# Kernel optimization log

Measured on AMD Instinct MI355X. Metric: run time of the kernel, lower is better.

The kernel has to match this reference:

```python
import jax, jax.numpy as jnp
import numpy as np

N = 100000      # nodes
E = 1600000     # edges
F_IN = 64       # CFG.feature_dim
H = 128         # CFG.hidden_dim
G = 128         # graphs in batch
LN_EPS = 1e-5


def setup_inputs() -> dict:
    key = jax.random.key(0)
    ks = jax.random.split(key, 12)
    x = jax.random.normal(ks[0], (N, F_IN), dtype=jnp.float32)
    edge_index = jax.random.randint(ks[1], (2, E), 0, N)
    batch = jnp.sort(jax.random.randint(ks[2], (N,), 0, G))
    # GCNConv weights (glorot-ish scale) and biases
    W1 = jax.random.normal(ks[3], (F_IN, H), dtype=jnp.float32) * (1.0 / np.sqrt(F_IN))
    b1 = jnp.zeros((H,), jnp.float32)
    W2 = jax.random.normal(ks[4], (H, H), dtype=jnp.float32) * (1.0 / np.sqrt(H))
    b2 = jnp.zeros((H,), jnp.float32)
    # LayerNorm affine params
    g1 = jnp.ones((H,), jnp.float32)
    beta1 = jnp.zeros((H,), jnp.float32)
    g2 = jnp.ones((H,), jnp.float32)
    beta2 = jnp.zeros((H,), jnp.float32)
    return {"x": x, "edge_index": edge_index, "batch": batch,
            "W1": W1, "b1": b1, "g1": g1, "beta1": beta1,
            "W2": W2, "b2": b2, "g2": g2, "beta2": beta2,
            "num_graphs": G}


def _gcn_conv(h, W, b, src, dst, n):
    """PyG GCNConv: add self-loops, symmetric D^-1/2 (A+I) D^-1/2 (h W) + b."""
    hw = h @ W                                   # [n, out]
    loop = jnp.arange(n, dtype=src.dtype)
    s = jnp.concatenate([src, loop])             # [E+n]
    d = jnp.concatenate([dst, loop])
    deg = jax.ops.segment_sum(jnp.ones_like(s, jnp.float32), d, num_segments=n)
    dinv = jax.lax.rsqrt(jnp.maximum(deg, 1e-12))
    norm = dinv[s] * dinv[d]                     # [E+n]
    msg = hw[s] * norm[:, None]                  # gather + scale
    out = jax.ops.segment_sum(msg, d, num_segments=n)
    return out + b


def _layer_norm(h, gamma, beta):
    mu = jnp.mean(h, axis=-1, keepdims=True)
    var = jnp.mean(jnp.square(h - mu), axis=-1, keepdims=True)
    return (h - mu) * jax.lax.rsqrt(var + LN_EPS) * gamma + beta


def reference(x, edge_index, batch, W1, b1, g1, beta1, W2, b2, g2, beta2, num_graphs):
    src, dst = edge_index[0], edge_index[1]
    n = x.shape[0]
    h = _gcn_conv(x, W1, b1, src, dst, n)
    h = _layer_norm(h, g1, beta1)
    h = jax.nn.relu(h)
    h = _gcn_conv(h, W2, b2, src, dst, n)
    h = _layer_norm(h, g2, beta2)
    # is_inverted defaults to False -> no sign flip
    sums = jax.ops.segment_sum(h, batch, num_segments=num_graphs)      # [G, H]
    counts = jax.ops.segment_sum(jnp.ones((n,), jnp.float32), batch, num_segments=num_graphs)
    return sums / jnp.maximum(counts, 1.0)[:, None]
```

## Files before the change

### kernel.cpp

```cpp
#include <hip/hip_runtime.h>

#define LN_EPS 1e-5f

typedef __attribute__((ext_vector_type(8))) short short8v;
typedef __attribute__((ext_vector_type(4))) float float4v;

__device__ __forceinline__ float bflo(unsigned u) { return __uint_as_float(u << 16); }
__device__ __forceinline__ float bfhi(unsigned u) { return __uint_as_float(u & 0xffff0000u); }
__device__ __forceinline__ unsigned short f2bf(float f) {
    unsigned b = __float_as_uint(f);
    unsigned r = b + 0x7fffu + ((b >> 16) & 1u);
    return (unsigned short)(r >> 16);
}
__device__ __forceinline__ unsigned pack2(float x, float y) {
    return (unsigned)f2bf(x) | ((unsigned)f2bf(y) << 16);
}
__device__ __forceinline__ void add8(float* a, uint4 u) {
    a[0] += bflo(u.x); a[1] += bfhi(u.x);
    a[2] += bflo(u.y); a[3] += bfhi(u.y);
    a[4] += bflo(u.z); a[5] += bfhi(u.z);
    a[6] += bflo(u.w); a[7] += bfhi(u.w);
}

union U4S8 { uint4 u; short8v s; };


#define CHUNK 4096
#define NBMAX 512
#define CSRCAP 8192

__launch_bounds__(256)
__global__ void k_bcnt(const int* __restrict__ dst, int e, int* __restrict__ bcnt) {
    __shared__ int hist[NBMAX];
    int tid = threadIdx.x;
    int c0 = blockIdx.x * CHUNK;
    if (c0 >= e) return;
    int cnt = min(CHUNK, e - c0);
    for (int t = tid; t < NBMAX; t += 256) hist[t] = 0;
    __syncthreads();
    for (int t = tid; t < cnt; t += 256)
        atomicAdd(&hist[((unsigned)dst[c0 + t]) >> 8], 1);
    __syncthreads();
    for (int b = tid; b < NBMAX; b += 256) {
        int h = hist[b];
        if (h > 0) atomicAdd(&bcnt[b], h);
    }
}

__launch_bounds__(512)
__global__ void k_bscan(const int* __restrict__ bcnt, int* __restrict__ bptr) {
    __shared__ int s[NBMAX];
    int tid = threadIdx.x;
    int v = bcnt[tid];
    s[tid] = v; __syncthreads();
    for (int o = 1; o < NBMAX; o <<= 1) {
        int t = (tid >= o) ? s[tid - o] : 0;
        __syncthreads();
        s[tid] += t;
        __syncthreads();
    }
    bptr[tid + 1] = s[tid];
    if (tid == 0) bptr[0] = 0;
}

__launch_bounds__(256)
__global__ void k_bucket(const int* __restrict__ src, const int* __restrict__ dst, int e,
                         const int* __restrict__ bptr, int* __restrict__ gcnt,
                         uint2* __restrict__ stage) {
    __shared__ uint2 ebuf[CHUNK];
    __shared__ int hist[NBMAX];
    __shared__ int base[NBMAX];
    int tid = threadIdx.x;
    int c0 = blockIdx.x * CHUNK;
    if (c0 >= e) return;
    int cnt = min(CHUNK, e - c0);

    for (int t = tid; t < NBMAX; t += 256) hist[t] = 0;
    __syncthreads();
    for (int t = tid; t < cnt; t += 256) {
        uint2 ed = make_uint2((unsigned)src[c0 + t], (unsigned)dst[c0 + t]);
        ebuf[t] = ed;
        atomicAdd(&hist[ed.y >> 8], 1);
    }
    __syncthreads();
    for (int b = tid; b < NBMAX; b += 256) {
        int h = hist[b];
        if (h > 0) base[b] = bptr[b] + atomicAdd(&gcnt[b], h);
    }
    __syncthreads();
    for (int t = tid; t < cnt; t += 256) {
        uint2 ed = ebuf[t];
        int p = atomicAdd(&base[ed.y >> 8], 1);
        stage[p] = ed;
    }
}

__launch_bounds__(256)
__global__ void k_csr(const uint2* __restrict__ stage, const int* __restrict__ bptr,
                      int* __restrict__ csr_src, int* __restrict__ row_ptr,
                      float* __restrict__ dinv, int n, int e) {
    __shared__ int cntl[256];
    __shared__ int sc[256];
    __shared__ int excl[256];
    __shared__ int cbuf[CSRCAP];
    int b = blockIdx.x;
    int lo = b << 8;
    int nn = min(n - lo, 256);
    int tid = threadIdx.x;
    int s0 = bptr[b], s1 = bptr[b + 1];
    int cntB = s1 - s0;

    cntl[tid] = 0;
    __syncthreads();
    for (int t = tid; t < cntB; t += 256) {
        int dl = (int)stage[s0 + t].y - lo;
        atomicAdd(&cntl[dl], 1);
    }
    __syncthreads();
    int deg = (tid < nn) ? cntl[tid] : 0;
    sc[tid] = deg; __syncthreads();
    for (int o = 1; o < 256; o <<= 1) {
        int t = (tid >= o) ? sc[tid - o] : 0;
        __syncthreads();
        sc[tid] += t;
        __syncthreads();
    }
    excl[tid] = sc[tid] - deg;
    if (tid < nn) {
        row_ptr[lo + tid] = s0 + excl[tid];
        dinv[lo + tid] = rsqrtf((float)(deg + 1));
    }
    if (b == 0 && tid == 0) row_ptr[n] = e;
    cntl[tid] = 0;
    __syncthreads();
    for (int t = tid; t < cntB; t += 256) {
        uint2 ed = stage[s0 + t];
        int dl = (int)ed.y - lo;
        int r = atomicAdd(&cntl[dl], 1);
        int p = excl[dl] + r;
        if (p < CSRCAP) cbuf[p] = (int)ed.x;
        else csr_src[s0 + p] = (int)ed.x;
    }
    __syncthreads();
    int lim = min(cntB, CSRCAP);
    for (int t = tid; t < lim; t += 256) csr_src[s0 + t] = cbuf[t];
}


__global__ void k_f2bs(const float* __restrict__ in, const float* __restrict__ dinv,
                       unsigned* __restrict__ out, int nu) {
    int i = blockIdx.x * blockDim.x + threadIdx.x;
    if (i < nu) {
        float2 v = ((const float2*)in)[i];
        float d = dinv[i >> 5];
        out[i] = pack2(v.x * d, v.y * d);
    }
}


__global__ void k_agg64b(const uint4* __restrict__ x4, const float* __restrict__ dinv,
                         const int* __restrict__ row_ptr, const int* __restrict__ csr_src,
                         uint4* __restrict__ out4, int n) {
    int lane = threadIdx.x & 63;
    int g = lane >> 3, c = lane & 7;
    int wid = (blockIdx.x * blockDim.x + threadIdx.x) >> 6;
    int nw = (gridDim.x * blockDim.x) >> 6;
    for (int i = wid; i < n; i += nw) {
        float a[8] = {0.f, 0.f, 0.f, 0.f, 0.f, 0.f, 0.f, 0.f};
        if (g == 0) {
            uint4 su = x4[(size_t)i * 8 + c];
            add8(a, su);
        }
        int j0 = row_ptr[i], j1 = row_ptr[i + 1];
        int j = j0 + g;
        for (; j + 8 < j1; j += 16) {
            int s0 = csr_src[j], s1 = csr_src[j + 8];
            uint4 u0 = x4[(size_t)s0 * 8 + c];
            uint4 u1 = x4[(size_t)s1 * 8 + c];
            add8(a, u0);
            add8(a, u1);
        }
        if (j < j1) {
            int s0 = csr_src[j];
            uint4 u0 = x4[(size_t)s0 * 8 + c];
            add8(a, u0);
        }
        #pragma unroll
        for (int k = 0; k < 8; ++k) {
            a[k] += __shfl_xor(a[k], 8);
            a[k] += __shfl_xor(a[k], 16);
            a[k] += __shfl_xor(a[k], 32);
        }
        if (g == 0) {
            float di = dinv[i];
            uint4 o;
            o.x = pack2(a[0] * di, a[1] * di);
            o.y = pack2(a[2] * di, a[3] * di);
            o.z = pack2(a[4] * di, a[5] * di);
            o.w = pack2(a[6] * di, a[7] * di);
            out4[(size_t)i * 8 + c] = o;
        }
    }
}

__global__ void k_agg128b(const uint4* __restrict__ h4, const float* __restrict__ dinv,
                          const int* __restrict__ row_ptr, const int* __restrict__ csr_src,
                          uint4* __restrict__ out4, int n) {
    int lane = threadIdx.x & 63;
    int q = lane >> 4, c = lane & 15;
    int wid = (blockIdx.x * blockDim.x + threadIdx.x) >> 6;
    int nw = (gridDim.x * blockDim.x) >> 6;
    for (int i = wid; i < n; i += nw) {
        float a[8] = {0.f, 0.f, 0.f, 0.f, 0.f, 0.f, 0.f, 0.f};
        if (q == 0) {
            uint4 su = h4[(size_t)i * 16 + c];
            add8(a, su);
        }
        int j0 = row_ptr[i], j1 = row_ptr[i + 1];
        int j = j0 + q;
        for (; j + 12 < j1; j += 16) {
            int s0 = csr_src[j], s1 = csr_src[j + 4];
            int s2 = csr_src[j + 8], s3 = csr_src[j + 12];
            uint4 u0 = h4[(size_t)s0 * 16 + c];
            uint4 u1 = h4[(size_t)s1 * 16 + c];
            uint4 u2 = h4[(size_t)s2 * 16 + c];
            uint4 u3 = h4[(size_t)s3 * 16 + c];
            add8(a, u0);
            add8(a, u1);
            add8(a, u2);
            add8(a, u3);
        }
        for (; j < j1; j += 4) {
            int s0 = csr_src[j];
            uint4 u0 = h4[(size_t)s0 * 16 + c];
            add8(a, u0);
        }
        #pragma unroll
        for (int k = 0; k < 8; ++k) {
            a[k] += __shfl_xor(a[k], 16);
            a[k] += __shfl_xor(a[k], 32);
        }
        if (q == 0) {
            float di = dinv[i];
            uint4 o;
            o.x = pack2(a[0] * di, a[1] * di);
            o.y = pack2(a[2] * di, a[3] * di);
            o.z = pack2(a[4] * di, a[5] * di);
            o.w = pack2(a[6] * di, a[7] * di);
            out4[(size_t)i * 16 + c] = o;
        }
    }
}


__launch_bounds__(256)
__global__ void k_mm1(const unsigned* __restrict__ aggb, const float* __restrict__ W1,
                      const float* __restrict__ b1, const float* __restrict__ g1,
                      const float* __restrict__ be1, const float* __restrict__ dinv,
                      unsigned short* __restrict__ hbs, int ntiles) {
    int lane = threadIdx.x & 63;
    int wv = threadIdx.x >> 6;
    int wpb = blockDim.x >> 6;
    int lc = lane & 15, lg = lane >> 4;

    short8v B[2][8];
    #pragma unroll
    for (int ks = 0; ks < 2; ++ks)
        #pragma unroll
        for (int cb = 0; cb < 8; ++cb) {
            short8v f;
            #pragma unroll
            for (int j = 0; j < 8; ++j) {
                int k = ks * 32 + lg * 8 + j;
                f[j] = (short)f2bf(W1[k * 128 + cb * 16 + lc]);
            }
            B[ks][cb] = f;
        }
    float bs[8], gm[8], bt[8];
    #pragma unroll
    for (int cb = 0; cb < 8; ++cb) {
        bs[cb] = b1[cb * 16 + lc];
        gm[cb] = g1[cb * 16 + lc];
        bt[cb] = be1[cb * 16 + lc];
    }

    for (int t = blockIdx.x * wpb + wv; t < ntiles; t += gridDim.x * wpb) {
        size_t arow = (size_t)(t * 16 + lc) * 32;
        U4S8 a0, a1;
        a0.u = *(const uint4*)&aggb[arow + lg * 4];
        a1.u = *(const uint4*)&aggb[arow + 16 + lg * 4];
        float4v acc[8];
        #pragma unroll
        for (int cb = 0; cb < 8; ++cb) acc[cb] = (float4v){0.f, 0.f, 0.f, 0.f};
        #pragma unroll
        for (int cb = 0; cb < 8; ++cb) {
            acc[cb] = __builtin_amdgcn_mfma_f32_16x16x32_bf16(a0.s, B[0][cb], acc[cb], 0, 0, 0);
            acc[cb] = __builtin_amdgcn_mfma_f32_16x16x32_bf16(a1.s, B[1][cb], acc[cb], 0, 0, 0);
        }
        #pragma unroll
        for (int reg = 0; reg < 4; ++reg) {
            float s = 0.f;
            #pragma unroll
            for (int cb = 0; cb < 8; ++cb) { acc[cb][reg] += bs[cb]; s += acc[cb][reg]; }
            s += __shfl_xor(s, 1); s += __shfl_xor(s, 2);
            s += __shfl_xor(s, 4); s += __shfl_xor(s, 8);
            float mu = s * (1.f / 128.f);
            float q = 0.f;
            #pragma unroll
            for (int cb = 0; cb < 8; ++cb) { float e = acc[cb][reg] - mu; q += e * e; }
            q += __shfl_xor(q, 1); q += __shfl_xor(q, 2);
            q += __shfl_xor(q, 4); q += __shfl_xor(q, 8);
            float rstd = rsqrtf(q * (1.f / 128.f) + LN_EPS);
            int rowi = t * 16 + lg * 4 + reg;
            float di = dinv[rowi];
            size_t row = (size_t)rowi * 128;
            #pragma unroll
            for (int cb = 0; cb < 8; ++cb) {
                float o = fmaf((acc[cb][reg] - mu) * rstd, gm[cb], bt[cb]);
                hbs[row + cb * 16 + lc] = f2bf(fmaxf(o, 0.f) * di);
            }
        }
    }
}

__launch_bounds__(256)
__global__ void k_mm2p(const unsigned* __restrict__ aggb, const float* __restrict__ W2,
                       const float* __restrict__ b2, const float* __restrict__ g2,
                       const float* __restrict__ be2, const int* __restrict__ batch,
                       float* __restrict__ psum, int ntiles) {
    __shared__ uint4 sB[4 * 8 * 64];
    for (int idx = threadIdx.x; idx < 2048; idx += blockDim.x) {
        int l = idx & 63;
        int f = idx >> 6;
        int ks = f >> 3, cb = f & 7;
        int kb = ks * 32 + (l >> 4) * 8;
        int col = cb * 16 + (l & 15);
        float p[8];
        #pragma unroll
        for (int j = 0; j < 8; ++j) p[j] = W2[(kb + j) * 128 + col];
        uint4 v;
        v.x = pack2(p[0], p[1]); v.y = pack2(p[2], p[3]);
        v.z = pack2(p[4], p[5]); v.w = pack2(p[6], p[7]);
        sB[idx] = v;
    }
    __syncthreads();

    int lane = threadIdx.x & 63;
    int wv = threadIdx.x >> 6;
    int wpb = blockDim.x >> 6;
    int lc = lane & 15, lg = lane >> 4;
    float bs[8], gm[8], bt[8];
    #pragma unroll
    for (int cb = 0; cb < 8; ++cb) {
        bs[cb] = b2[cb * 16 + lc];
        gm[cb] = g2[cb * 16 + lc];
        bt[cb] = be2[cb * 16 + lc];
    }

    for (int t = blockIdx.x * wpb + wv; t < ntiles; t += gridDim.x * wpb) {
        int row0 = t * 16;
        size_t arow = (size_t)(row0 + lc) * 64;
        U4S8 a[4];
        #pragma unroll
        for (int ks = 0; ks < 4; ++ks)
            a[ks].u = *(const uint4*)&aggb[arow + ks * 16 + lg * 4];
        float4v acc[8];
        #pragma unroll
        for (int cb = 0; cb < 8; ++cb) acc[cb] = (float4v){0.f, 0.f, 0.f, 0.f};
        #pragma unroll
        for (int ks = 0; ks < 4; ++ks) {
            #pragma unroll
            for (int cb = 0; cb < 8; ++cb) {
                U4S8 fb;
                fb.u = sB[(ks * 8 + cb) * 64 + lane];
                acc[cb] = __builtin_amdgcn_mfma_f32_16x16x32_bf16(a[ks].s, fb.s, acc[cb], 0, 0, 0);
            }
        }
        #pragma unroll
        for (int reg = 0; reg < 4; ++reg) {
            float s = 0.f;
            #pragma unroll
            for (int cb = 0; cb < 8; ++cb) { acc[cb][reg] += bs[cb]; s += acc[cb][reg]; }
            s += __shfl_xor(s, 1); s += __shfl_xor(s, 2);
            s += __shfl_xor(s, 4); s += __shfl_xor(s, 8);
            float mu = s * (1.f / 128.f);
            float q = 0.f;
            #pragma unroll
            for (int cb = 0; cb < 8; ++cb) { float e = acc[cb][reg] - mu; q += e * e; }
            q += __shfl_xor(q, 1); q += __shfl_xor(q, 2);
            q += __shfl_xor(q, 4); q += __shfl_xor(q, 8);
            float rstd = rsqrtf(q * (1.f / 128.f) + LN_EPS);
            #pragma unroll
            for (int cb = 0; cb < 8; ++cb)
                acc[cb][reg] = fmaf((acc[cb][reg] - mu) * rstd, gm[cb], bt[cb]);
        }
        int gmin = batch[row0];
        int gmax = batch[row0 + 15];
        int rg[4];
        #pragma unroll
        for (int reg = 0; reg < 4; ++reg) rg[reg] = batch[row0 + lg * 4 + reg];
        for (int g = gmin; g <= gmax; ++g) {
            #pragma unroll
            for (int cb = 0; cb < 8; ++cb) {
                float s = 0.f;
                #pragma unroll
                for (int reg = 0; reg < 4; ++reg)
                    s += (rg[reg] == g) ? acc[cb][reg] : 0.f;
                s += __shfl_xor(s, 16);
                s += __shfl_xor(s, 32);
                if (lg == 0) atomicAdd(&psum[g * 128 + cb * 16 + lc], s);
            }
        }
    }
}


__device__ __forceinline__ int lowerb(const int* __restrict__ b, int n, int key) {
    int lo = 0, hi = n;
    while (lo < hi) {
        int m = (lo + hi) >> 1;
        if (b[m] < key) lo = m + 1; else hi = m;
    }
    return lo;
}

__global__ void k_div(float* __restrict__ out, const int* __restrict__ batch,
                      int n, int total) {
    int idx = blockIdx.x * blockDim.x + threadIdx.x;
    if (idx < total) {
        int g = idx >> 7;
        int start = lowerb(batch, n, g);
        int end   = lowerb(batch, n, g + 1);
        out[idx] /= fmaxf((float)(end - start), 1.f);
    }
}


extern "C" void kernel_launch(void* const* d_in, const int* in_sizes, int n_in,
                              void* d_out, int out_size, void* d_ws, size_t ws_size,
                              hipStream_t stream) {
    const float* x   = (const float*)d_in[0];
    const int*   ei  = (const int*)d_in[1];
    const int*   bat = (const int*)d_in[2];
    const float* W1  = (const float*)d_in[3];
    const float* b1  = (const float*)d_in[4];
    const float* g1  = (const float*)d_in[5];
    const float* be1 = (const float*)d_in[6];
    const float* W2  = (const float*)d_in[7];
    const float* b2  = (const float*)d_in[8];
    const float* g2  = (const float*)d_in[9];
    const float* be2 = (const float*)d_in[10];

    int n = in_sizes[0] / 64;
    int e = in_sizes[1] / 2;
    const int* src = ei;
    const int* dst = ei + e;

    char* ws = (char*)d_ws;
    size_t off = 0;
    auto take = [&](size_t bytes) -> void* {
        void* p = ws + off;
        off = (off + bytes + 255) & ~(size_t)255;
        return p;
    };
    float*    dinv    = (float*)   take((size_t)n * 4);
    int*      row_ptr = (int*)     take((size_t)(n + 1) * 4);
    int*      bcnt    = (int*)     take(NBMAX * 4);
    int*      bptr    = (int*)     take((NBMAX + 1) * 4);
    int*      gcnt    = (int*)     take(NBMAX * 4);
    uint2*    stage   = (uint2*)   take((size_t)e * 8);
    int*      csr_src = (int*)     take((size_t)e * 4);
    unsigned* xb      = (unsigned*)take((size_t)n * 64 * 2);
    unsigned* aggb    = (unsigned*)take((size_t)n * 64 * 2);
    unsigned* hb      = (unsigned*)take((size_t)n * 128 * 2);
    unsigned* agg2b   = (unsigned*)take((size_t)n * 128 * 2);

    hipMemsetAsync(bcnt, 0, NBMAX * 4, stream);
    hipMemsetAsync(gcnt, 0, NBMAX * 4, stream);
    hipMemsetAsync(d_out, 0, (size_t)out_size * 4, stream);

    int nbk = (e + CHUNK - 1) / CHUNK;
    k_bcnt<<<nbk, 256, 0, stream>>>(dst, e, bcnt);
    k_bscan<<<1, NBMAX, 0, stream>>>(bcnt, bptr);
    k_bucket<<<nbk, 256, 0, stream>>>(src, dst, e, bptr, gcnt, stage);
    int nbuckets = (n + 255) / 256;
    k_csr<<<nbuckets, 256, 0, stream>>>(stage, bptr, csr_src, row_ptr, dinv, n, e);

    int nux = n * 32;
    k_f2bs<<<(nux + 255) / 256, 256, 0, stream>>>(x, dinv, xb, nux);

    k_agg64b<<<2048, 256, 0, stream>>>((const uint4*)xb, dinv, row_ptr, csr_src,
                                       (uint4*)aggb, n);

    int ntiles = n / 16;
    int mmblocks = (ntiles + 3) / 4;
    k_mm1<<<mmblocks, 256, 0, stream>>>(aggb, W1, b1, g1, be1, dinv,
                                        (unsigned short*)hb, ntiles);

    k_agg128b<<<2048, 256, 0, stream>>>((const uint4*)hb, dinv, row_ptr, csr_src,
                                        (uint4*)agg2b, n);

    k_mm2p<<<mmblocks, 256, 0, stream>>>(agg2b, W2, b2, g2, be2, bat, (float*)d_out, ntiles);

    int total = out_size;
    k_div<<<(total + 255) / 256, 256, 0, stream>>>((float*)d_out, bat, n, total);
}
```

Measured before the change: 233.3 us.

## Pack staged edges into 32 bits, fuse LayerNorm stats, use HIP bf16 intrinsics

Staged edges are now packed into one 32-bit word: the source index in the low 24 bits and the destination's offset within its 256-node bucket in the top 8 bits. This halves staging traffic between the bucketing and CSR kernels. Both LayerNorm epilogues now compute the sum and the sum of squares in a single pass with interleaved shuffles, instead of a separate variance pass. The bf16 conversion switches to the HIP library intrinsics. The packing assumes node indices fit in 24 bits, and the single-pass variance may be less numerically robust.

```diff
diff --git a/kernel.cpp b/kernel.cpp
--- a/kernel.cpp
+++ b/kernel.cpp
@@ -1,4 +1,5 @@
 #include <hip/hip_runtime.h>
+#include <hip/hip_bf16.h>
 
 #define LN_EPS 1e-5f
 
@@ -8,12 +9,12 @@
 __device__ __forceinline__ float bflo(unsigned u) { return __uint_as_float(u << 16); }
 __device__ __forceinline__ float bfhi(unsigned u) { return __uint_as_float(u & 0xffff0000u); }
 __device__ __forceinline__ unsigned short f2bf(float f) {
-    unsigned b = __float_as_uint(f);
-    unsigned r = b + 0x7fffu + ((b >> 16) & 1u);
-    return (unsigned short)(r >> 16);
+    __hip_bfloat16 b = __float2bfloat16(f);
+    return *reinterpret_cast<unsigned short*>(&b);
 }
 __device__ __forceinline__ unsigned pack2(float x, float y) {
-    return (unsigned)f2bf(x) | ((unsigned)f2bf(y) << 16);
+    __hip_bfloat162 t = __float22bfloat162_rn(make_float2(x, y));
+    return *reinterpret_cast<unsigned*>(&t);
 }
 __device__ __forceinline__ void add8(float* a, uint4 u) {
     a[0] += bflo(u.x); a[1] += bfhi(u.x);
@@ -66,8 +67,9 @@
 __launch_bounds__(256)
 __global__ void k_bucket(const int* __restrict__ src, const int* __restrict__ dst, int e,
                          const int* __restrict__ bptr, int* __restrict__ gcnt,
-                         uint2* __restrict__ stage) {
-    __shared__ uint2 ebuf[CHUNK];
+                         unsigned* __restrict__ stage) {
+    __shared__ unsigned ebuf[CHUNK];
+    __shared__ unsigned short ebkt[CHUNK];
     __shared__ int hist[NBMAX];
     __shared__ int base[NBMAX];
     int tid = threadIdx.x;
@@ -78,9 +80,11 @@
     for (int t = tid; t < NBMAX; t += 256) hist[t] = 0;
     __syncthreads();
     for (int t = tid; t < cnt; t += 256) {
-        uint2 ed = make_uint2((unsigned)src[c0 + t], (unsigned)dst[c0 + t]);
-        ebuf[t] = ed;
-        atomicAdd(&hist[ed.y >> 8], 1);
+        unsigned s = (unsigned)src[c0 + t];
+        unsigned d = (unsigned)dst[c0 + t];
+        ebuf[t] = s | ((d & 0xffu) << 24);
+        ebkt[t] = (unsigned short)(d >> 8);
+        atomicAdd(&hist[d >> 8], 1);
     }
     __syncthreads();
     for (int b = tid; b < NBMAX; b += 256) {
@@ -89,14 +93,13 @@
     }
     __syncthreads();
     for (int t = tid; t < cnt; t += 256) {
-        uint2 ed = ebuf[t];
-        int p = atomicAdd(&base[ed.y >> 8], 1);
-        stage[p] = ed;
+        int p = atomicAdd(&base[ebkt[t]], 1);
+        stage[p] = ebuf[t];
     }
 }
 
 __launch_bounds__(256)
-__global__ void k_csr(const uint2* __restrict__ stage, const int* __restrict__ bptr,
+__global__ void k_csr(const unsigned* __restrict__ stage, const int* __restrict__ bptr,
                       int* __restrict__ csr_src, int* __restrict__ row_ptr,
                       float* __restrict__ dinv, int n, int e) {
     __shared__ int cntl[256];
@@ -113,7 +116,7 @@
     cntl[tid] = 0;
     __syncthreads();
     for (int t = tid; t < cntB; t += 256) {
-        int dl = (int)stage[s0 + t].y - lo;
+        int dl = (int)(stage[s0 + t] >> 24);
         atomicAdd(&cntl[dl], 1);
     }
     __syncthreads();
@@ -134,12 +137,12 @@
     cntl[tid] = 0;
     __syncthreads();
     for (int t = tid; t < cntB; t += 256) {
-        uint2 ed = stage[s0 + t];
-        int dl = (int)ed.y - lo;
+        unsigned ed = stage[s0 + t];
+        int dl = (int)(ed >> 24);
         int r = atomicAdd(&cntl[dl], 1);
         int p = excl[dl] + r;
-        if (p < CSRCAP) cbuf[p] = (int)ed.x;
-        else csr_src[s0 + p] = (int)ed.x;
+        if (p < CSRCAP) cbuf[p] = (int)(ed & 0x00ffffffu);
+        else csr_src[s0 + p] = (int)(ed & 0x00ffffffu);
     }
     __syncthreads();
     int lim = min(cntB, CSRCAP);
@@ -299,18 +302,20 @@
         }
         #pragma unroll
         for (int reg = 0; reg < 4; ++reg) {
-            float s = 0.f;
-            #pragma unroll
-            for (int cb = 0; cb < 8; ++cb) { acc[cb][reg] += bs[cb]; s += acc[cb][reg]; }
-            s += __shfl_xor(s, 1); s += __shfl_xor(s, 2);
-            s += __shfl_xor(s, 4); s += __shfl_xor(s, 8);
+            float s = 0.f, q = 0.f;
+            #pragma unroll
+            for (int cb = 0; cb < 8; ++cb) {
+                float v = acc[cb][reg] + bs[cb];
+                acc[cb][reg] = v;
+                s += v; q = fmaf(v, v, q);
+            }
+            s += __shfl_xor(s, 1); q += __shfl_xor(q, 1);
+            s += __shfl_xor(s, 2); q += __shfl_xor(q, 2);
+            s += __shfl_xor(s, 4); q += __shfl_xor(q, 4);
+            s += __shfl_xor(s, 8); q += __shfl_xor(q, 8);
             float mu = s * (1.f / 128.f);
-            float q = 0.f;
-            #pragma unroll
-            for (int cb = 0; cb < 8; ++cb) { float e = acc[cb][reg] - mu; q += e * e; }
-            q += __shfl_xor(q, 1); q += __shfl_xor(q, 2);
-            q += __shfl_xor(q, 4); q += __shfl_xor(q, 8);
-            float rstd = rsqrtf(q * (1.f / 128.f) + LN_EPS);
+            float var = fmaf(q, 1.f / 128.f, -mu * mu);
+            float rstd = rsqrtf(var + LN_EPS);
             int rowi = t * 16 + lg * 4 + reg;
             float di = dinv[rowi];
             size_t row = (size_t)rowi * 128;
@@ -378,18 +383,20 @@
         }
         #pragma unroll
         for (int reg = 0; reg < 4; ++reg) {
-            float s = 0.f;
-            #pragma unroll
-            for (int cb = 0; cb < 8; ++cb) { acc[cb][reg] += bs[cb]; s += acc[cb][reg]; }
-            s += __shfl_xor(s, 1); s += __shfl_xor(s, 2);
-            s += __shfl_xor(s, 4); s += __shfl_xor(s, 8);
+            float s = 0.f, q = 0.f;
+            #pragma unroll
+            for (int cb = 0; cb < 8; ++cb) {
+                float v = acc[cb][reg] + bs[cb];
+                acc[cb][reg] = v;
+                s += v; q = fmaf(v, v, q);
+            }
+            s += __shfl_xor(s, 1); q += __shfl_xor(q, 1);
+            s += __shfl_xor(s, 2); q += __shfl_xor(q, 2);
+            s += __shfl_xor(s, 4); q += __shfl_xor(q, 4);
+            s += __shfl_xor(s, 8); q += __shfl_xor(q, 8);
             float mu = s * (1.f / 128.f);
-            float q = 0.f;
-            #pragma unroll
-            for (int cb = 0; cb < 8; ++cb) { float e = acc[cb][reg] - mu; q += e * e; }
-            q += __shfl_xor(q, 1); q += __shfl_xor(q, 2);
-            q += __shfl_xor(q, 4); q += __shfl_xor(q, 8);
-            float rstd = rsqrtf(q * (1.f / 128.f) + LN_EPS);
+            float var = fmaf(q, 1.f / 128.f, -mu * mu);
+            float rstd = rsqrtf(var + LN_EPS);
             #pragma unroll
             for (int cb = 0; cb < 8; ++cb)
                 acc[cb][reg] = fmaf((acc[cb][reg] - mu) * rstd, gm[cb], bt[cb]);
@@ -468,7 +475,7 @@
     int*      bcnt    = (int*)     take(NBMAX * 4);
     int*      bptr    = (int*)     take((NBMAX + 1) * 4);
     int*      gcnt    = (int*)     take(NBMAX * 4);
-    uint2*    stage   = (uint2*)   take((size_t)e * 8);
+    unsigned* stage   = (unsigned*)take((size_t)e * 4);
     int*      csr_src = (int*)     take((size_t)e * 4);
     unsigned* xb      = (unsigned*)take((size_t)n * 64 * 2);
     unsigned* aggb    = (unsigned*)take((size_t)n * 64 * 2);
```

New measurement: 226.8 us. 2.8% less time.
